# Kernel tuning notes

Measured on AMD Instinct MI355X. Metric: run time of the kernel, lower is better.

Reference implementation:

```python
import jax, jax.numpy as jnp
import numpy as np

N, E, DIN, DOUT, DE = 100000, 250000, 32, 32, 13


def setup_inputs() -> dict:
    key = jax.random.key(0)
    ks = jax.random.split(key, 10)
    def u(k, shape, fan):
        b = 1.0 / np.sqrt(fan)
        return jax.random.uniform(k, shape, jnp.float32, -b, b)
    x = jax.random.normal(ks[0], (N, DIN), jnp.float32)
    edge_index = jax.random.randint(ks[1], (2, E), 0, N)
    edge_attr = jax.random.uniform(ks[2], (E, DE), jnp.float32)
    # NNConv's edge network: Linear(DE -> DIN*DOUT)
    nn_w = u(ks[3], (DIN * DOUT, DE), DE)
    nn_b = u(ks[4], (DIN * DOUT,), DE)
    # NNConv root weight + bias
    root = u(ks[5], (DIN, DOUT), DIN)
    bias = jnp.zeros((DOUT,), jnp.float32)
    # GRU(input=DIN, hidden=DOUT), single layer, seq_len=1
    w_ih = u(ks[6], (3 * DOUT, DIN), DOUT)
    w_hh = u(ks[7], (3 * DOUT, DOUT), DOUT)
    b_ih = u(ks[8], (3 * DOUT,), DOUT)
    b_hh = u(ks[9], (3 * DOUT,), DOUT)
    return dict(x=x, edge_attr=edge_attr, nn_w=nn_w, nn_b=nn_b, root=root,
                bias=bias, w_ih=w_ih, w_hh=w_hh, b_ih=b_ih, b_hh=b_hh,
                edge_index=edge_index)


def reference(x, edge_attr, nn_w, nn_b, root, bias, w_ih, w_hh, b_ih, b_hh, edge_index):
    identity = x
    h0 = x  # h is None -> h = x.unsqueeze(0); squeeze the seq dim here
    # norm='_None' (identity) and Dropout in eval mode (identity)
    src, dst = edge_index[0], edge_index[1]
    # NNConv: per-edge weight matrix from edge_attr  [E, DIN, DOUT]
    W = (edge_attr @ nn_w.T + nn_b).reshape(E, DIN, DOUT)
    msg = jnp.einsum('ei,eio->eo', x[src], W)           # [E, DOUT]
    agg = jax.ops.segment_sum(msg, dst, num_segments=N)  # [N, DOUT]
    cnt = jax.ops.segment_sum(jnp.ones((E, 1), x.dtype), dst, num_segments=N)
    mean = agg / jnp.maximum(cnt, 1.0)                   # aggr='mean'
    conv = mean + x @ root + bias
    # celu then GRU step (seq_len=1)
    c = jax.nn.celu(conv)
    gi = c @ w_ih.T + b_ih
    gh = h0 @ w_hh.T + b_hh
    ir, iz, ic = jnp.split(gi, 3, axis=1)
    hr, hz, hc = jnp.split(gh, 3, axis=1)
    r = jax.nn.sigmoid(ir + hr)
    z = jax.nn.sigmoid(iz + hz)
    n = jnp.tanh(ic + r * hc)
    h_new = (1.0 - z) * n + z * h0
    out = jax.nn.relu(h_new + identity)  # res=True, act=ReLU
    return out, h_new[None]
```

## Files before the change

### kernel.cpp

```cpp
#include <hip/hip_runtime.h>
#include <hip/hip_bf16.h>
#include <stdint.h>

#define DIN 32
#define DOUT 32
#define DE 13

typedef float f32x4 __attribute__((ext_vector_type(4)));
typedef short s16x8 __attribute__((ext_vector_type(8)));
typedef int   i32x4 __attribute__((ext_vector_type(4)));
typedef unsigned int u32x4 __attribute__((ext_vector_type(4)));

__device__ __forceinline__ float bf2f(unsigned short u) {
    return __uint_as_float(((uint32_t)u) << 16);
}
__device__ __forceinline__ unsigned short f2bf(float f) {
    uint32_t b = __float_as_uint(f);
    b += 0x7FFFu + ((b >> 16) & 1u);
    return (unsigned short)(b >> 16);
}
__device__ __forceinline__ uint32_t pk2(float a, float b) {
    float2 t; t.x = a; t.y = b;
    __hip_bfloat162 h = __float22bfloat162_rn(t);
    return *(uint32_t*)&h;
}
__device__ __forceinline__ float sigm(float v) { return 1.f / (1.f + __expf(-v)); }
__device__ __forceinline__ float tanh_fast(float v) { return 2.f / (1.f + __expf(-2.f * v)) - 1.f; }

#define KE_LDS (28 * 512)
__global__ __launch_bounds__(256, 4) void kE(const float* __restrict__ x,
        const float* __restrict__ ea, const int* __restrict__ ei,
        const float* __restrict__ nn_w, const float* __restrict__ nn_b,
        uint32_t* __restrict__ agg, float* __restrict__ cnt, int E) {
    __shared__ unsigned short Al[KE_LDS];
    __shared__ uint32_t trD[4][2][256];
    const int tid = threadIdx.x;
    for (int t = tid; t < KE_LDS; t += 256) {
        int j = t & 7;
        int lane = (t >> 3) & 63;
        int tile = t >> 9;
        int at2 = tile >= 14 ? 1 : 0;
        int kt = tile - at2 * 14;
        int o = at2 * 16 + (lane & 15);
        int i = ((lane >> 4) << 3) + j;
        float v = (kt < 13) ? nn_w[(i * 32 + o) * 13 + kt] : nn_b[i * 32 + o];
        Al[t] = f2bf(v);
    }
    __syncthreads();
    const int lane = tid & 63;
    const int wv = tid >> 6;
    const int el = lane & 15;
    const int quad = lane >> 4;
    const int q8 = quad << 3;
    const int wave = (blockIdx.x * 256 + tid) >> 6;
    const int nw = (gridDim.x * 256) >> 6;
    const int nstrips = E >> 4;
    int sC = wave;
    if (sC >= nstrips) return;
    int sN = sC + nw, sNN = sN + nw;

    const int eC = (sC << 4) + el;
    const int srcC = ei[eC];
    int dstC = ei[E + eC];
    int srcN = 0, dstN = 0;
    if (sN < nstrips) {
        const int e1 = (sN << 4) + el;
        srcN = ei[e1];
        dstN = ei[E + e1];
    }
    {
        const float* eab = ea + (size_t)(sC << 4) * 13;
        #pragma unroll
        for (int t = 0; t < 4; ++t) {
            int idx = t * 64 + lane;
            if (idx < 208) trD[wv][0][idx] = __float_as_uint(eab[idx]);
        }
    }
    uint32_t eaR[4] = {0u, 0u, 0u, 0u};
    if (sN < nstrips) {
        const float* eab = ea + (size_t)(sN << 4) * 13;
        #pragma unroll
        for (int t = 0; t < 4; ++t) {
            int idx = t * 64 + lane;
            eaR[t] = (idx < 208) ? __float_as_uint(eab[idx]) : 0u;
        }
    }
    const float* xq0 = x + (size_t)srcC * 32 + q8;
    f32x4 xlo = *(const f32x4*)xq0;
    f32x4 xhi = *(const f32x4*)(xq0 + 4);

    int pb = 0;
    const f32x4 zz = {0.f, 0.f, 0.f, 0.f};
    for (;;) {
        const bool hasN  = sN  < nstrips;
        const bool hasNN = sNN < nstrips;
        int srcNN = 0, dstNN = 0;
        if (hasNN) {
            const int e2 = (sNN << 4) + el;
            srcNN = ei[e2];
            dstNN = ei[E + e2];
        }
        if (hasN) {
            #pragma unroll
            for (int t = 0; t < 4; ++t) {
                int idx = t * 64 + lane;
                if (idx < 208) trD[wv][pb ^ 1][idx] = eaR[t];
            }
        }
        if (hasNN) {
            const float* eab = ea + (size_t)(sNN << 4) * 13;
            #pragma unroll
            for (int t = 0; t < 4; ++t) {
                int idx = t * 64 + lane;
                eaR[t] = (idx < 208) ? __float_as_uint(eab[idx]) : 0u;
            }
        }
        i32x4 bi;
        bi[0] = pk2(xlo[0], xlo[1]);
        bi[1] = pk2(xlo[2], xlo[3]);
        bi[2] = pk2(xhi[0], xhi[1]);
        bi[3] = pk2(xhi[2], xhi[3]);
        s16x8 bfr = __builtin_bit_cast(s16x8, bi);
        s16x8 aB0 = *(const s16x8*)&Al[13 * 512 + lane * 8];
        s16x8 aB1 = *(const s16x8*)&Al[27 * 512 + lane * 8];
        f32x4 acc0 = __builtin_amdgcn_mfma_f32_16x16x32_bf16(aB0, bfr, zz, 0, 0, 0);
        f32x4 acc1 = __builtin_amdgcn_mfma_f32_16x16x32_bf16(aB1, bfr, zz, 0, 0, 0);
        #pragma unroll
        for (int kt = 0; kt < 13; ++kt) {
            s16x8 a0 = *(const s16x8*)&Al[kt * 512 + lane * 8];
            s16x8 a1 = *(const s16x8*)&Al[(14 + kt) * 512 + lane * 8];
            f32x4 y0 = __builtin_amdgcn_mfma_f32_16x16x32_bf16(a0, bfr, zz, 0, 0, 0);
            f32x4 y1 = __builtin_amdgcn_mfma_f32_16x16x32_bf16(a1, bfr, zz, 0, 0, 0);
            float gk = __uint_as_float(trD[wv][pb][el * 13 + kt]);
            #pragma unroll
            for (int r = 0; r < 4; ++r) {
                acc0[r] = fmaf(gk, y0[r], acc0[r]);
                acc1[r] = fmaf(gk, y1[r], acc1[r]);
            }
        }
        {
            u32x4 pw;
            pw[0] = pk2(acc0[0], acc1[0]);
            pw[1] = pk2(acc0[1], acc1[1]);
            pw[2] = pk2(acc0[2], acc1[2]);
            pw[3] = pk2(acc0[3], acc1[3]);
            *(u32x4*)&trD[wv][pb][el * 16 + quad * 4] = pw;
        }
        uint32_t v4s[4];
        int dd[4];
        #pragma unroll
        for (int p = 0; p < 4; ++p) {
            int e4 = (p << 2) + quad;
            v4s[p] = trD[wv][pb][e4 * 16 + el];
            dd[p] = __shfl(dstC, e4, 64);
        }
        if (hasN) {
            const float* xq = x + (size_t)srcN * 32 + q8;
            xlo = *(const f32x4*)xq;
            xhi = *(const f32x4*)(xq + 4);
        }
        __builtin_amdgcn_sched_barrier(0);
        #pragma unroll
        for (int p = 0; p < 4; ++p) {
            __hip_bfloat162 hv = *(__hip_bfloat162*)&v4s[p];
            unsafeAtomicAdd((__hip_bfloat162*)&agg[(size_t)dd[p] * 16 + el], hv);
        }
        if (lane < 16) atomicAdd(&cnt[dstC], 1.0f);
        __builtin_amdgcn_sched_barrier(0);
        if (!hasN) break;
        sC = sN; sN = sNN; sNN += nw;
        dstC = dstN; srcN = srcNN; dstN = dstNN;
        pb ^= 1;
    }
}

__global__ __launch_bounds__(256, 4) void kF(const float* __restrict__ x,
        const uint32_t* __restrict__ aggw, const float* __restrict__ cnt,
        const float* __restrict__ root, const float* __restrict__ bias,
        const float* __restrict__ w_ih, const float* __restrict__ w_hh,
        const float* __restrict__ b_ih, const float* __restrict__ b_hh,
        float* __restrict__ out, float* __restrict__ hnew, int N) {
    __shared__ __align__(16) char smem[30720];
    unsigned short* Bl = (unsigned short*)smem;
    float* scr = (float*)(smem + 14336);
    unsigned short* clds = (unsigned short*)(smem + 14336);
    const int tid = threadIdx.x;
    {
        *(f32x4*)&scr[tid * 4] = *(const f32x4*)&root[tid * 4];
        #pragma unroll
        for (int it = 0; it < 3; ++it)
            *(f32x4*)&scr[1024 + it * 1024 + tid * 4] =
                *(const f32x4*)&w_hh[it * 1024 + tid * 4];
    }
    __syncthreads();
    for (int t = tid; t < 8 * 512; t += 256) {
        int j = t & 7;
        int ln = (t >> 3) & 63;
        int tt = t >> 9;
        int i = ((ln >> 4) << 3) + j;
        int c = ln & 15;
        int col = tt * 16 + c;
        float v = (col < 32) ? scr[i * 32 + col] : scr[1024 + (col - 32) * 32 + i];
        Bl[t] = f2bf(v);
    }
    __syncthreads();
    #pragma unroll
    for (int it = 0; it < 3; ++it)
        *(f32x4*)&scr[it * 1024 + tid * 4] = *(const f32x4*)&w_ih[it * 1024 + tid * 4];
    __syncthreads();
    for (int t = tid + 8 * 512; t < 14 * 512; t += 256) {
        int j = t & 7;
        int ln = (t >> 3) & 63;
        int tt = t >> 9;
        int i = ((ln >> 4) << 3) + j;
        int c = ln & 15;
        Bl[t] = f2bf(scr[((tt - 8) * 16 + c) * 32 + i]);
    }
    __syncthreads();
    const int lane = tid & 63;
    const int wv = tid >> 6;
    const int c15 = lane & 15;
    const int rowb = (lane >> 4) << 2;
    unsigned short* cl = clds + wv * 512;
    float binit[14];
    #pragma unroll
    for (int t = 0; t < 2; ++t) binit[t] = bias[t * 16 + c15];
    #pragma unroll
    for (int t = 2; t < 8; ++t) binit[t] = b_hh[t * 16 + c15 - 32];
    #pragma unroll
    for (int u = 0; u < 6; ++u) binit[8 + u] = b_ih[u * 16 + c15];
    int wave = (blockIdx.x * 256 + tid) >> 6;
    const int nw = (gridDim.x * 256) >> 6;
    const int nstrips = N >> 4;
    for (int s = wave; s < nstrips; s += nw) {
        const int n0 = s << 4;
        const float* xp = x + (size_t)(n0 + c15) * 32 + ((lane >> 4) << 3);
        f32x4 x0 = *(const f32x4*)xp;
        f32x4 x1 = *(const f32x4*)(xp + 4);
        float xr[4][2], ag[4][2], cn[4];
        #pragma unroll
        for (int r = 0; r < 4; ++r) {
            const int n = n0 + rowb + r;
            uint32_t w = aggw[(size_t)n * 16 + c15];
            ag[r][0] = bf2f((unsigned short)(w & 0xFFFFu));
            ag[r][1] = bf2f((unsigned short)(w >> 16));
            cn[r] = cnt[n];
            #pragma unroll
            for (int t = 0; t < 2; ++t)
                xr[r][t] = x[(size_t)n * 32 + t * 16 + c15];
        }
        s16x8 a;
        a[0] = (short)f2bf(x0[0]); a[1] = (short)f2bf(x0[1]);
        a[2] = (short)f2bf(x0[2]); a[3] = (short)f2bf(x0[3]);
        a[4] = (short)f2bf(x1[0]); a[5] = (short)f2bf(x1[1]);
        a[6] = (short)f2bf(x1[2]); a[7] = (short)f2bf(x1[3]);
        f32x4 D[8];
        #pragma unroll
        for (int t = 0; t < 8; ++t) {
            s16x8 b = *(const s16x8*)&Bl[(t * 64 + lane) * 8];
            f32x4 ci = {binit[t], binit[t], binit[t], binit[t]};
            D[t] = __builtin_amdgcn_mfma_f32_16x16x32_bf16(a, b, ci, 0, 0, 0);
        }
        #pragma unroll
        for (int r = 0; r < 4; ++r) {
            float icn = 1.f / fmaxf(cn[r], 1.f);
            #pragma unroll
            for (int t = 0; t < 2; ++t) {
                float conv = ag[r][t] * icn + D[t][r];
                float cv = conv > 0.f ? conv : (__expf(conv) - 1.f);
                cl[(rowb + r) * 32 + t * 16 + c15] = f2bf(cv);
            }
        }
        s16x8 a2 = *(const s16x8*)&cl[c15 * 32 + ((lane >> 4) << 3)];
        f32x4 G[6];
        #pragma unroll
        for (int u = 0; u < 6; ++u) {
            s16x8 b = *(const s16x8*)&Bl[((8 + u) * 64 + lane) * 8];
            f32x4 ci = {binit[8 + u], binit[8 + u], binit[8 + u], binit[8 + u]};
            G[u] = __builtin_amdgcn_mfma_f32_16x16x32_bf16(a2, b, ci, 0, 0, 0);
        }
        #pragma unroll
        for (int t = 0; t < 2; ++t) {
            #pragma unroll
            for (int r = 0; r < 4; ++r) {
                float rg = sigm(G[t][r] + D[2 + t][r]);
                float z  = sigm(G[2 + t][r] + D[4 + t][r]);
                float nn = tanh_fast(G[4 + t][r] + rg * D[6 + t][r]);
                float h  = (1.f - z) * nn + z * xr[r][t];
                float ov = h + xr[r][t];
                size_t oi = (size_t)(n0 + rowb + r) * 32 + t * 16 + c15;
                out[oi]  = ov > 0.f ? ov : 0.f;
                hnew[oi] = h;
            }
        }
    }
}

extern "C" void kernel_launch(void* const* d_in, const int* in_sizes, int n_in,
                              void* d_out, int out_size, void* d_ws, size_t ws_size,
                              hipStream_t stream) {
    const float* x    = (const float*)d_in[0];
    const float* ea   = (const float*)d_in[1];
    const float* nn_w = (const float*)d_in[2];
    const float* nn_b = (const float*)d_in[3];
    const float* root = (const float*)d_in[4];
    const float* bias = (const float*)d_in[5];
    const float* w_ih = (const float*)d_in[6];
    const float* w_hh = (const float*)d_in[7];
    const float* b_ih = (const float*)d_in[8];
    const float* b_hh = (const float*)d_in[9];
    const int*   ei   = (const int*)d_in[10];
    const int N = in_sizes[0] / DIN;
    const int E = in_sizes[10] / 2;
    float* out  = (float*)d_out;
    float* hnew = out + (size_t)N * DOUT;

    const size_t agg_bytes = (size_t)N * 16 * sizeof(uint32_t);

    uint32_t* agg = (uint32_t*)d_ws;
    float* cnt = (float*)((char*)d_ws + agg_bytes);
    kE<<<1024, 256, 0, stream>>>(x, ea, ei, nn_w, nn_b, agg, cnt, E);
    kF<<<1024, 256, 0, stream>>>(x, agg, cnt, root, bias,
                                 w_ih, w_hh, b_ih, b_hh, out, hnew, N);
}
```

Before: 147.8 us.

## Replace atomic scatter-add with counting-sort bucketed messages and gather-reduce

Instead of bf16 atomic adds into a per-node accumulator, the edge kernel now writes each message to a destination-bucketed slot. The slot positions come from a histogram kernel and a block-scan kernel that computes per-node base offsets. The node kernel then sums each node's messages sequentially, which removes the contention of bf16 packed atomics and gives an fp32 sum. In exchange it adds two kernel launches, a memset, an E*64-byte message buffer, a per-edge atomicSub, and divergent per-node loops in the node kernel.

```diff
diff --git a/kernel.cpp b/kernel.cpp
--- a/kernel.cpp
+++ b/kernel.cpp
@@ -27,11 +27,50 @@
 __device__ __forceinline__ float sigm(float v) { return 1.f / (1.f + __expf(-v)); }
 __device__ __forceinline__ float tanh_fast(float v) { return 2.f / (1.f + __expf(-2.f * v)) - 1.f; }
 
+
+__global__ __launch_bounds__(256) void kH(const int* __restrict__ ei,
+                                          int* __restrict__ cntI, int E) {
+    int e = blockIdx.x * 256 + threadIdx.x;
+    if (e < E) atomicAdd(&cntI[ei[E + e]], 1);
+}
+
+__global__ __launch_bounds__(1024) void kA(const int* __restrict__ cntI,
+        int* __restrict__ base, float* __restrict__ degF,
+        unsigned int* __restrict__ gtot, int N) {
+    __shared__ int wsum[16];
+    __shared__ unsigned int bbase;
+    const int tid = threadIdx.x;
+    const int lane = tid & 63;
+    const int wv = tid >> 6;
+    const int n = blockIdx.x * 1024 + tid;
+    int d = (n < N) ? cntI[n] : 0;
+    int sc = d;
+    #pragma unroll
+    for (int o = 1; o < 64; o <<= 1) {
+        int t = __shfl_up(sc, o, 64);
+        if (lane >= o) sc += t;
+    }
+    if (lane == 63) wsum[wv] = sc;
+    __syncthreads();
+    if (tid == 0) {
+        int tot = 0;
+        #pragma unroll
+        for (int w = 0; w < 16; ++w) { int t = wsum[w]; wsum[w] = tot; tot += t; }
+        bbase = atomicAdd(gtot, (unsigned int)tot);
+    }
+    __syncthreads();
+    if (n < N) {
+        base[n] = (int)bbase + wsum[wv] + (sc - d);
+        degF[n] = (float)d;
+    }
+}
+
 #define KE_LDS (28 * 512)
 __global__ __launch_bounds__(256, 4) void kE(const float* __restrict__ x,
         const float* __restrict__ ea, const int* __restrict__ ei,
         const float* __restrict__ nn_w, const float* __restrict__ nn_b,
-        uint32_t* __restrict__ agg, float* __restrict__ cnt, int E) {
+        uint32_t* __restrict__ msg, const int* __restrict__ base,
+        int* __restrict__ cntI, int E) {
     __shared__ unsigned short Al[KE_LDS];
     __shared__ uint32_t trD[4][2][256];
     const int tid = threadIdx.x;
@@ -61,7 +100,7 @@
 
     const int eC = (sC << 4) + el;
     const int srcC = ei[eC];
-    int dstC = ei[E + eC];
+    const int dstC = ei[E + eC];
     int srcN = 0, dstN = 0;
     if (sN < nstrips) {
         const int e1 = (sN << 4) + el;
@@ -88,6 +127,9 @@
     const float* xq0 = x + (size_t)srcC * 32 + q8;
     f32x4 xlo = *(const f32x4*)xq0;
     f32x4 xhi = *(const f32x4*)(xq0 + 4);
+    int posC = 0;
+    if (lane < 16)
+        posC = base[dstC] + atomicSub(&cntI[dstC], 1) - 1;
 
     int pb = 0;
     const f32x4 zz = {0.f, 0.f, 0.f, 0.f};
@@ -115,6 +157,9 @@
                 eaR[t] = (idx < 208) ? __float_as_uint(eab[idx]) : 0u;
             }
         }
+        int posN = 0;
+        if (hasN && lane < 16)
+            posN = base[dstN] + atomicSub(&cntI[dstN], 1) - 1;
         i32x4 bi;
         bi[0] = pk2(xlo[0], xlo[1]);
         bi[1] = pk2(xlo[2], xlo[3]);
@@ -147,12 +192,12 @@
             *(u32x4*)&trD[wv][pb][el * 16 + quad * 4] = pw;
         }
         uint32_t v4s[4];
-        int dd[4];
+        int pp[4];
         #pragma unroll
         for (int p = 0; p < 4; ++p) {
             int e4 = (p << 2) + quad;
             v4s[p] = trD[wv][pb][e4 * 16 + el];
-            dd[p] = __shfl(dstC, e4, 64);
+            pp[p] = __shfl(posC, e4, 64);
         }
         if (hasN) {
             const float* xq = x + (size_t)srcN * 32 + q8;
@@ -161,21 +206,20 @@
         }
         __builtin_amdgcn_sched_barrier(0);
         #pragma unroll
-        for (int p = 0; p < 4; ++p) {
-            __hip_bfloat162 hv = *(__hip_bfloat162*)&v4s[p];
-            unsafeAtomicAdd((__hip_bfloat162*)&agg[(size_t)dd[p] * 16 + el], hv);
-        }
-        if (lane < 16) atomicAdd(&cnt[dstC], 1.0f);
+        for (int p = 0; p < 4; ++p)
+            msg[(size_t)pp[p] * 16 + el] = v4s[p];
         __builtin_amdgcn_sched_barrier(0);
         if (!hasN) break;
         sC = sN; sN = sNN; sNN += nw;
-        dstC = dstN; srcN = srcNN; dstN = dstNN;
+        srcN = srcNN; dstN = dstNN;
+        posC = posN;
         pb ^= 1;
     }
 }
 
 __global__ __launch_bounds__(256, 4) void kF(const float* __restrict__ x,
-        const uint32_t* __restrict__ aggw, const float* __restrict__ cnt,
+        const uint32_t* __restrict__ msg, const int* __restrict__ base,
+        const float* __restrict__ degF,
         const float* __restrict__ root, const float* __restrict__ bias,
         const float* __restrict__ w_ih, const float* __restrict__ w_hh,
         const float* __restrict__ b_ih, const float* __restrict__ b_hh,
@@ -237,17 +281,26 @@
         const float* xp = x + (size_t)(n0 + c15) * 32 + ((lane >> 4) << 3);
         f32x4 x0 = *(const f32x4*)xp;
         f32x4 x1 = *(const f32x4*)(xp + 4);
-        float xr[4][2], ag[4][2], cn[4];
+        int bs[4]; float dg[4]; float xr[4][2], ag[4][2];
         #pragma unroll
         for (int r = 0; r < 4; ++r) {
             const int n = n0 + rowb + r;
-            uint32_t w = aggw[(size_t)n * 16 + c15];
-            ag[r][0] = bf2f((unsigned short)(w & 0xFFFFu));
-            ag[r][1] = bf2f((unsigned short)(w >> 16));
-            cn[r] = cnt[n];
-            #pragma unroll
-            for (int t = 0; t < 2; ++t)
-                xr[r][t] = x[(size_t)n * 32 + t * 16 + c15];
+            bs[r] = base[n];
+            dg[r] = degF[n];
+            xr[r][0] = x[(size_t)n * 32 + c15];
+            xr[r][1] = x[(size_t)n * 32 + 16 + c15];
+        }
+        #pragma unroll
+        for (int r = 0; r < 4; ++r) {
+            float a0 = 0.f, a1 = 0.f;
+            const int dgi = (int)dg[r];
+            const uint32_t* mp = msg + (size_t)bs[r] * 16 + c15;
+            for (int j = 0; j < dgi; ++j) {
+                uint32_t w = mp[j * 16];
+                a0 += bf2f((unsigned short)(w & 0xFFFFu));
+                a1 += bf2f((unsigned short)(w >> 16));
+            }
+            ag[r][0] = a0; ag[r][1] = a1;
         }
         s16x8 a;
         a[0] = (short)f2bf(x0[0]); a[1] = (short)f2bf(x0[1]);
@@ -263,7 +316,7 @@
         }
         #pragma unroll
         for (int r = 0; r < 4; ++r) {
-            float icn = 1.f / fmaxf(cn[r], 1.f);
+            float icn = 1.f / fmaxf(dg[r], 1.f);
             #pragma unroll
             for (int t = 0; t < 2; ++t) {
                 float conv = ag[r][t] * icn + D[t][r];
@@ -315,11 +368,17 @@
     float* out  = (float*)d_out;
     float* hnew = out + (size_t)N * DOUT;
 
-    const size_t agg_bytes = (size_t)N * 16 * sizeof(uint32_t);
-
-    uint32_t* agg = (uint32_t*)d_ws;
-    float* cnt = (float*)((char*)d_ws + agg_bytes);
-    kE<<<1024, 256, 0, stream>>>(x, ea, ei, nn_w, nn_b, agg, cnt, E);
-    kF<<<1024, 256, 0, stream>>>(x, agg, cnt, root, bias,
+    uint32_t* msg  = (uint32_t*)d_ws;
+    char* p1 = (char*)d_ws + (size_t)E * 64;
+    int*   base = (int*)p1;
+    float* degF = (float*)(p1 + (size_t)N * 4);
+    int*   cntI = (int*)(p1 + (size_t)N * 8);
+    unsigned int* gtot = (unsigned int*)(p1 + (size_t)N * 12);
+
+    hipMemsetAsync(cntI, 0, (size_t)N * 4 + 4, stream);
+    kH<<<(E + 255) / 256, 256, 0, stream>>>(ei, cntI, E);
+    kA<<<(N + 1023) / 1024, 1024, 0, stream>>>(cntI, base, degF, gtot, N);
+    kE<<<1024, 256, 0, stream>>>(x, ea, ei, nn_w, nn_b, msg, base, cntI, E);
+    kF<<<1024, 256, 0, stream>>>(x, msg, base, degF, root, bias,
                                  w_ih, w_hh, b_ih, b_hh, out, hnew, N);
 }
```

After: 171.2 us. 15.9% more time.
